# Optimization experiments

Hardware: AMD Instinct MI355X
Metric: run time of the kernel (lower is better)

Reference implementation:

```python
import jax, jax.numpy as jnp
import numpy as np

D_MODEL = 1024
N_HEADS = 16
HEAD_DIM = D_MODEL // N_HEADS  # 64
BATCH, SEQ = 2, 2048
MASK_FILL = -1000000000.0


def setup_inputs() -> dict:
    key = jax.random.key(0)
    ks = jax.random.split(key, 13)
    s = 1.0 / np.sqrt(D_MODEL)
    inp = {
        "q": jax.random.normal(ks[0], (BATCH, SEQ, D_MODEL), jnp.float32),
        "k": jax.random.normal(ks[1], (BATCH, SEQ, D_MODEL), jnp.float32),
        "v": jax.random.normal(ks[2], (BATCH, SEQ, D_MODEL), jnp.float32),
        "mask": jax.random.randint(ks[3], (BATCH, 1, SEQ, SEQ), 0, 2, jnp.int32),
        "Wq": jax.random.normal(ks[4], (D_MODEL, D_MODEL), jnp.float32) * s,
        "bq": jax.random.normal(ks[5], (D_MODEL,), jnp.float32) * s,
        "Wk": jax.random.normal(ks[6], (D_MODEL, D_MODEL), jnp.float32) * s,
        "bk": jax.random.normal(ks[7], (D_MODEL,), jnp.float32) * s,
        "Wv": jax.random.normal(ks[8], (D_MODEL, D_MODEL), jnp.float32) * s,
        "bv": jax.random.normal(ks[9], (D_MODEL,), jnp.float32) * s,
        "Wo": jax.random.normal(ks[10], (D_MODEL, D_MODEL), jnp.float32) * s,
        "bo": jax.random.normal(ks[11], (D_MODEL,), jnp.float32) * s,
    }
    return inp


def reference(q, k, v, mask, Wq, bq, Wk, bk, Wv, bv, Wo, bo):
    batch, seq, feat = q.shape
    # Linear projections (torch Linear: x @ W.T + b)
    qp = q @ Wq.T + bq
    kp = k @ Wk.T + bk
    vp = v @ Wv.T + bv

    def split(x):
        # (B, S, D) -> (B, H, S, Dh)
        return x.reshape(batch, seq, N_HEADS, HEAD_DIM).swapaxes(1, 2)

    qh, kh, vh = split(qp), split(kp), split(vp)

    # (B, H, S, S) score matrix, scaled
    score = jnp.einsum("bhqd,bhkd->bhqk", qh, kh) / jnp.sqrt(
        jnp.asarray(HEAD_DIM, qh.dtype))
    score = jnp.where(mask == 0, jnp.asarray(MASK_FILL, score.dtype), score)
    attn = jax.nn.softmax(score, axis=-1)
    out = jnp.einsum("bhqk,bhkd->bhqd", attn, vh)  # (B, H, S, Dh)
    joint = out.swapaxes(1, 2).reshape(batch, seq, feat)
    return joint @ Wo.T + bo
```

## Files before the change

kernel.cpp:

```cpp
#include <hip/hip_runtime.h>

typedef unsigned short u16;
typedef unsigned long long u64;
typedef float f32x4 __attribute__((ext_vector_type(4)));
typedef __bf16 bf16x4 __attribute__((ext_vector_type(4)));
typedef __bf16 bf16x8 __attribute__((ext_vector_type(8)));
typedef u16 u16x8 __attribute__((ext_vector_type(8)));

#define QSCALE 0.18033688011112042f

__device__ __forceinline__ u16 f2bf(float f) {
  unsigned int u = __float_as_uint(f);
  u += 0x7fffu + ((u >> 16) & 1u);
  return (u16)(u >> 16);
}

__device__ __forceinline__ void async16(const void* g, void* l) {
  __builtin_amdgcn_global_load_lds(
      (__attribute__((address_space(1))) void*)g,
      (__attribute__((address_space(3))) void*)l,
      16, 0, 0);
}

__device__ __forceinline__ f32x4 mfma16(bf16x8 a, bf16x8 b, f32x4 c) {
  return __builtin_amdgcn_mfma_f32_16x16x32_bf16(a, b, c, 0, 0, 0);
}

struct CvtArgs {
  const float* src[7];
  u16* dst[7];
};

__global__ __launch_bounds__(256) void cvt_kernel(CvtArgs a) {
  int z = blockIdx.z;
  int n = (z < 3) ? 4194304 : 1048576;
  int base = (blockIdx.x * 256 + threadIdx.x) * 8;
  if (base >= n) return;
  const float* s = a.src[z] + base;
  f32x4 x0 = *(const f32x4*)s;
  f32x4 x1 = *(const f32x4*)(s + 4);
  u16x8 pk;
  pk[0]=f2bf(x0[0]); pk[1]=f2bf(x0[1]); pk[2]=f2bf(x0[2]); pk[3]=f2bf(x0[3]);
  pk[4]=f2bf(x1[0]); pk[5]=f2bf(x1[1]); pk[6]=f2bf(x1[2]); pk[7]=f2bf(x1[3]);
  *(u16x8*)(a.dst[z] + base) = pk;
}

__global__ __launch_bounds__(256) void pack_mask_kernel(
    const int* __restrict__ mask, u64* __restrict__ pm) {
  int idx = blockIdx.x * 256 + threadIdx.x;
  const int4* src = (const int4*)(mask + (size_t)idx * 64);
  u64 bits = 0ull;
#pragma unroll
  for (int j = 0; j < 16; ++j) {
    int4 v = src[j];
    if (v.x) bits |= 1ull << (4 * j + 0);
    if (v.y) bits |= 1ull << (4 * j + 1);
    if (v.z) bits |= 1ull << (4 * j + 2);
    if (v.w) bits |= 1ull << (4 * j + 3);
  }
  pm[idx] = bits;
}

__device__ __forceinline__ void gemm_body(const u16* __restrict__ A,
                                          const u16* __restrict__ W,
                                          const float* __restrict__ bias,
                                          void* __restrict__ outraw, int mode,
                                          float oscale) {
  alignas(16) __shared__ u16 lA[128 * 32];
  alignas(16) __shared__ u16 lB[128 * 32];
  const int tid = threadIdx.x;
  const int lane = tid & 63, wv = tid >> 6;
  const int wm = wv >> 1, wn = wv & 1;
  const int m0 = blockIdx.y * 128, n0 = blockIdx.x * 128;
  const int l15 = lane & 15, quad = lane >> 4;
  const int srow = lane >> 2;
  const int scol = (lane & 3) * 8;

  f32x4 acc[4][4] = {};

  for (int k0 = 0; k0 < 1024; k0 += 32) {
#pragma unroll
    for (int t = 0; t < 2; ++t) {
      int rb = (wv * 2 + t) * 16;
      async16(A + (size_t)(m0 + rb + srow) * 1024 + k0 + scol, (char*)lA + rb * 64);
      async16(W + (size_t)(n0 + rb + srow) * 1024 + k0 + scol, (char*)lB + rb * 64);
    }
    __syncthreads();
    bf16x8 af[4], bfr[4];
#pragma unroll
    for (int i = 0; i < 4; ++i) {
      af[i]  = *(const bf16x8*)(lA + (wm * 64 + i * 16 + l15) * 32 + quad * 8);
      bfr[i] = *(const bf16x8*)(lB + (wn * 64 + i * 16 + l15) * 32 + quad * 8);
    }
#pragma unroll
    for (int i = 0; i < 4; ++i)
#pragma unroll
      for (int j = 0; j < 4; ++j)
        acc[i][j] = mfma16(af[i], bfr[j], acc[i][j]);
    __syncthreads();
  }

#pragma unroll
  for (int i = 0; i < 4; ++i) {
    int mbase = m0 + wm * 64 + i * 16 + quad * 4;
#pragma unroll
    for (int j = 0; j < 4; ++j) {
      int n = n0 + wn * 64 + j * 16 + l15;
      float bv = bias[n];
#pragma unroll
      for (int r = 0; r < 4; ++r) {
        int m = mbase + r;
        float val = (acc[i][j][r] + bv) * oscale;
        if (mode == 0) {
          int b = m >> 11, s = m & 2047, h = n >> 6, dh = n & 63;
          ((u16*)outraw)[((((size_t)b * 16 + h) * 2048 + s) << 6) + dh] = f2bf(val);
        } else if (mode == 1) {
          int b = m >> 11, s = m & 2047, h = n >> 6, dh = n & 63;
          ((u16*)outraw)[((((size_t)b * 16 + h) * 64 + dh) << 11) + s] = f2bf(val);
        } else {
          ((float*)outraw)[(size_t)m * 1024 + n] = val;
        }
      }
    }
  }
}

__global__ __launch_bounds__(256) void gemm_qkv_kernel(
    const u16* __restrict__ qb, const u16* __restrict__ kb, const u16* __restrict__ vb,
    const u16* __restrict__ Wqb, const float* __restrict__ bq,
    const u16* __restrict__ Wkb, const float* __restrict__ bk,
    const u16* __restrict__ Wvb, const float* __restrict__ bv,
    u16* __restrict__ qp, u16* __restrict__ kp, u16* __restrict__ vt) {
  if (blockIdx.z == 0)      gemm_body(qb, Wqb, bq, qp, 0, QSCALE);
  else if (blockIdx.z == 1) gemm_body(kb, Wkb, bk, kp, 0, 1.0f);
  else                      gemm_body(vb, Wvb, bv, vt, 1, 1.0f);
}

__global__ __launch_bounds__(256) void gemm_o_kernel(
    const u16* __restrict__ joint, const u16* __restrict__ Wob,
    const float* __restrict__ bo, float* __restrict__ out) {
  gemm_body(joint, Wob, bo, out, 2, 1.0f);
}

__global__ __launch_bounds__(256, 2) void attn_kernel(
    const u16* __restrict__ qp, const u16* __restrict__ kp,
    const u16* __restrict__ vt, const u64* __restrict__ pm,
    u16* __restrict__ joint) {
  alignas(16) __shared__ u16 kbuf[2][4096];
  alignas(16) __shared__ u16 vbuf[2][4096];
  alignas(16) __shared__ u16 pbuf[4][2][1024];

  const int tid = threadIdx.x, lane = tid & 63, wv = tid >> 6;
  const int quad = lane >> 4, l15 = lane & 15;
  const int q0 = blockIdx.x * 128;
  const int h = blockIdx.y, b = blockIdx.z;
  const size_t head_off = ((size_t)b * 16 + h) * 2048 * 64;
  const u16* Qh = qp + head_off;
  const u16* Kh = kp + head_off;
  const u16* Vh = vt + head_off;
  const int qr0 = q0 + wv * 32 + l15;
  const u64* pmq = pm + ((size_t)b * 2048 + qr0) * 32;

  bf16x8 qf[2][2];
#pragma unroll
  for (int g = 0; g < 2; ++g) {
    const u16* qrow = Qh + (size_t)(qr0 + g * 16) * 64 + quad * 8;
    qf[g][0] = *(const bf16x8*)(qrow);
    qf[g][1] = *(const bf16x8*)(qrow + 32);
  }

  const int sd0 = tid, sd1 = 256 + tid;
  const int snt0 = sd0 >> 7, shalf0 = (sd0 >> 6) & 1, sl60 = sd0 & 63;
  const int snt1 = sd1 >> 7, shalf1 = (sd1 >> 6) & 1, sl61 = sd1 & 63;
  const u16* kg0 = Kh + (size_t)(snt0 * 16 + (sl60 & 15)) * 64 + shalf0 * 32 + (sl60 >> 4) * 8;
  const u16* kg1 = Kh + (size_t)(snt1 * 16 + (sl61 & 15)) * 64 + shalf1 * 32 + (sl61 >> 4) * 8;
  const int vb0 = sd0 >> 6, vb1 = sd1 >> 6;
  const u16* vg0 = Vh + (size_t)((vb0 >> 1) * 16 + (sl60 & 15)) * 2048 + (vb0 & 1) * 32 + (sl60 >> 4) * 8;
  const u16* vg1 = Vh + (size_t)((vb1 >> 1) * 16 + (sl61 & 15)) * 2048 + (vb1 & 1) * 32 + (sl61 >> 4) * 8;

  f32x4 O[2][4] = {};
  f32x4 lacc[2] = {};
  const f32x4 fz = {};

  f32x4 SA[2][4], SB[2][4];
  bf16x8 vfA[8], vfB[8];
  u64 wA0, wA1, wB0, wB1;

#define SM_CHUNK(SP, WLO, WHI, g, nt)                                          \
  do {                                                                         \
    unsigned int hw_ = ((nt) < 2) ? (WLO) : (WHI);                             \
    unsigned int nib_ = hw_ >> (((nt) & 1) * 16 + quad * 4);                   \
    _Pragma("unroll") for (int r_ = 0; r_ < 4; ++r_) {                         \
      float pe_ = __builtin_amdgcn_exp2f(SP[g][nt][r_]);                       \
      SP[g][nt][r_] = ((nib_ >> r_) & 1u) ? pe_ : 0.f;                         \
    }                                                                          \
    lacc[g] += SP[g][nt];                                                      \
    bf16x4 pv_ = __builtin_convertvector(SP[g][nt], bf16x4);                   \
    int t4_ = 4 * (nt) + quad;                                                 \
    int ks_ = t4_ >> 3, qd_ = (t4_ & 7) >> 1;                                  \
    u16* pw_ = pbuf[wv][g] + ks_ * 512 + qd_ * 128 + l15 * 8 + (t4_ & 1) * 4;  \
    *(u64*)pw_ = *(const u64*)&pv_;                                            \
  } while (0)

#define ATTN_STEP(SC, SP, VC, VP, WC0, WC1, WP0, WP1, KT)                      \
  do {                                                                         \
    const int kt_ = (KT);                                                      \
    if (kt_ != 31) {                                                           \
      const size_t kadv_ = (size_t)(kt_ + 1) * 4096;                           \
      const int vadv_ = (kt_ + 1) * 64;                                        \
      char* kd_ = (char*)kbuf[(kt_ + 1) & 1];                                  \
      char* vd_ = (char*)vbuf[(kt_ + 1) & 1];                                  \
      async16(kg0 + kadv_, kd_ + sd0 * 16);                                    \
      async16(kg1 + kadv_, kd_ + sd1 * 16);                                    \
      async16(vg0 + vadv_, vd_ + sd0 * 16);                                    \
      async16(vg1 + vadv_, vd_ + sd1 * 16);                                    \
    }                                                                          \
    WC0 = pmq[kt_]; WC1 = pmq[kt_ + 512];                                      \
    const u16* kc_ = kbuf[kt_ & 1];                                            \
    const u16* vc_ = vbuf[kt_ & 1];                                            \
    unsigned int plo0_ = (unsigned int)(WP0), phi0_ = (unsigned int)((WP0) >> 32); \
    unsigned int plo1_ = (unsigned int)(WP1), phi1_ = (unsigned int)((WP1) >> 32); \
    _Pragma("unroll") for (int nt = 0; nt < 4; ++nt) {                         \
      bf16x8 k0_ = *(const bf16x8*)(kc_ + nt * 1024 + lane * 8);               \
      bf16x8 k1_ = *(const bf16x8*)(kc_ + nt * 1024 + 512 + lane * 8);         \
      f32x4 z0_ = mfma16(k0_, qf[0][0], fz);                                   \
      SC[0][nt] = mfma16(k1_, qf[0][1], z0_);                                  \
      f32x4 z1_ = mfma16(k0_, qf[1][0], fz);                                   \
      SC[1][nt] = mfma16(k1_, qf[1][1], z1_);                                  \
      SM_CHUNK(SP, plo0_, phi0_, 0, nt);                                       \
      SM_CHUNK(SP, plo1_, phi1_, 1, nt);                                       \
    }                                                                          \
    asm volatile("s_waitcnt lgkmcnt(0)" ::: "memory");                         \
    _Pragma("unroll") for (int ks = 0; ks < 2; ++ks) {                         \
      bf16x8 pf0_ = *(const bf16x8*)(pbuf[wv][0] + ks * 512 + lane * 8);       \
      bf16x8 pf1_ = *(const bf16x8*)(pbuf[wv][1] + ks * 512 + lane * 8);       \
      _Pragma("unroll") for (int nt = 0; nt < 4; ++nt) {                       \
        O[0][nt] = mfma16(VP[2 * nt + ks], pf0_, O[0][nt]);                    \
        O[1][nt] = mfma16(VP[2 * nt + ks], pf1_, O[1][nt]);                    \
      }                                                                        \
    }                                                                          \
    _Pragma("unroll") for (int nt = 0; nt < 4; ++nt) {                         \
      VC[2 * nt]     = *(const bf16x8*)(vc_ + (nt * 2) * 512 + lane * 8);      \
      VC[2 * nt + 1] = *(const bf16x8*)(vc_ + (nt * 2 + 1) * 512 + lane * 8);  \
    }                                                                          \
    __syncthreads();                                                           \
  } while (0)

  async16(kg0, (char*)kbuf[0] + sd0 * 16);
  async16(kg1, (char*)kbuf[0] + sd1 * 16);
  async16(vg0, (char*)vbuf[0] + sd0 * 16);
  async16(vg1, (char*)vbuf[0] + sd1 * 16);
  __syncthreads();

  async16(kg0 + 4096, (char*)kbuf[1] + sd0 * 16);
  async16(kg1 + 4096, (char*)kbuf[1] + sd1 * 16);
  async16(vg0 + 64,   (char*)vbuf[1] + sd0 * 16);
  async16(vg1 + 64,   (char*)vbuf[1] + sd1 * 16);

  wA0 = pmq[0]; wA1 = pmq[512];
#pragma unroll
  for (int nt = 0; nt < 4; ++nt) {
    bf16x8 k0_ = *(const bf16x8*)(kbuf[0] + nt * 1024 + lane * 8);
    bf16x8 k1_ = *(const bf16x8*)(kbuf[0] + nt * 1024 + 512 + lane * 8);
    f32x4 z0_ = mfma16(k0_, qf[0][0], fz);
    SA[0][nt] = mfma16(k1_, qf[0][1], z0_);
    f32x4 z1_ = mfma16(k0_, qf[1][0], fz);
    SA[1][nt] = mfma16(k1_, qf[1][1], z1_);
  }
#pragma unroll
  for (int nt = 0; nt < 4; ++nt) {
    vfA[2 * nt]     = *(const bf16x8*)(vbuf[0] + (nt * 2) * 512 + lane * 8);
    vfA[2 * nt + 1] = *(const bf16x8*)(vbuf[0] + (nt * 2 + 1) * 512 + lane * 8);
  }
  __syncthreads();

  for (int it = 0; it < 15; ++it) {
    ATTN_STEP(SB, SA, vfB, vfA, wB0, wB1, wA0, wA1, 2 * it + 1);
    ATTN_STEP(SA, SB, vfA, vfB, wA0, wA1, wB0, wB1, 2 * it + 2);
  }
  ATTN_STEP(SB, SA, vfB, vfA, wB0, wB1, wA0, wA1, 31);

  {
    unsigned int plo0_ = (unsigned int)wB0, phi0_ = (unsigned int)(wB0 >> 32);
    unsigned int plo1_ = (unsigned int)wB1, phi1_ = (unsigned int)(wB1 >> 32);
#pragma unroll
    for (int nt = 0; nt < 4; ++nt) {
      SM_CHUNK(SB, plo0_, phi0_, 0, nt);
      SM_CHUNK(SB, plo1_, phi1_, 1, nt);
    }
    asm volatile("s_waitcnt lgkmcnt(0)" ::: "memory");
#pragma unroll
    for (int ks = 0; ks < 2; ++ks) {
      bf16x8 pf0_ = *(const bf16x8*)(pbuf[wv][0] + ks * 512 + lane * 8);
      bf16x8 pf1_ = *(const bf16x8*)(pbuf[wv][1] + ks * 512 + lane * 8);
#pragma unroll
      for (int nt = 0; nt < 4; ++nt) {
        O[0][nt] = mfma16(vfB[2 * nt + ks], pf0_, O[0][nt]);
        O[1][nt] = mfma16(vfB[2 * nt + ks], pf1_, O[1][nt]);
      }
    }
  }

#undef ATTN_STEP
#undef SM_CHUNK

#pragma unroll
  for (int g = 0; g < 2; ++g) {
    float l = (lacc[g][0] + lacc[g][1]) + (lacc[g][2] + lacc[g][3]);
    l += __shfl_xor(l, 16, 64);
    l += __shfl_xor(l, 32, 64);
    float inv = 1.0f / l;
    size_t row_off = ((size_t)b * 2048 + qr0 + g * 16) * 1024 + h * 64;
#pragma unroll
    for (int nt = 0; nt < 4; ++nt) {
      f32x4 ov = O[g][nt] * inv;
      bf16x4 obv = __builtin_convertvector(ov, bf16x4);
      *(u64*)(joint + row_off + nt * 16 + quad * 4) = *(const u64*)&obv;
    }
  }
}

extern "C" void kernel_launch(void* const* d_in, const int* in_sizes, int n_in,
                              void* d_out, int out_size, void* d_ws, size_t ws_size,
                              hipStream_t stream) {
  const float* q  = (const float*)d_in[0];
  const float* k  = (const float*)d_in[1];
  const float* v  = (const float*)d_in[2];
  const int* mask = (const int*)d_in[3];
  const float* Wq = (const float*)d_in[4];
  const float* bq = (const float*)d_in[5];
  const float* Wk = (const float*)d_in[6];
  const float* bk = (const float*)d_in[7];
  const float* Wv = (const float*)d_in[8];
  const float* bv = (const float*)d_in[9];
  const float* Wo = (const float*)d_in[10];
  const float* bo = (const float*)d_in[11];
  float* out = (float*)d_out;

  u16* w = (u16*)d_ws;
  u16* qp    = w;
  u16* kp    = w + 4194304;
  u16* vt    = w + 8388608;
  u16* qb    = w + 12582912;
  u16* kb    = w + 16777216;
  u16* vb    = w + 20971520;
  u16* Wqb   = w + 25165824;
  u16* Wkb   = w + 26214400;
  u16* Wvb   = w + 27262976;
  u16* Wob   = w + 28311552;
  u64* pm    = (u64*)(w + 29360128);
  u16* joint = qb;

  CvtArgs ca;
  ca.src[0] = q;  ca.dst[0] = qb;
  ca.src[1] = k;  ca.dst[1] = kb;
  ca.src[2] = v;  ca.dst[2] = vb;
  ca.src[3] = Wq; ca.dst[3] = Wqb;
  ca.src[4] = Wk; ca.dst[4] = Wkb;
  ca.src[5] = Wv; ca.dst[5] = Wvb;
  ca.src[6] = Wo; ca.dst[6] = Wob;

  pack_mask_kernel<<<dim3(512), dim3(256), 0, stream>>>(mask, pm);
  cvt_kernel<<<dim3(2048, 1, 7), dim3(256), 0, stream>>>(ca);
  gemm_qkv_kernel<<<dim3(8, 32, 3), dim3(256), 0, stream>>>(
      qb, kb, vb, Wqb, bq, Wkb, bk, Wvb, bv, qp, kp, vt);
  attn_kernel<<<dim3(16, 16, 2), dim3(256), 0, stream>>>(qp, kp, vt, pm, joint);
  gemm_o_kernel<<<dim3(8, 32, 1), dim3(256), 0, stream>>>(joint, Wob, bo, out);
}
```

Before: 285.6 us.

## Load K/V fragments directly from global into registers, drop LDS staging and barriers

The attention kernel stops staging K and V tiles through shared memory with async global-to-LDS copies. Each wave now loads its own K and V MFMA fragments straight from global memory into registers, double-buffering K in registers, and the per-step __syncthreads is removed. This frees LDS and removes block-wide synchronisation, but each of the four waves now fetches the same K/V data separately. That multiplies global/L2 traffic, and V loads are strided by rows of 2048, which risks exposed load latency.

Result: slower. 348.7 us (+22.1%).

```diff
diff --git a/kernel.cpp b/kernel.cpp
--- a/kernel.cpp
+++ b/kernel.cpp
@@ -146,8 +146,6 @@
     const u16* __restrict__ qp, const u16* __restrict__ kp,
     const u16* __restrict__ vt, const u64* __restrict__ pm,
     u16* __restrict__ joint) {
-  alignas(16) __shared__ u16 kbuf[2][4096];
-  alignas(16) __shared__ u16 vbuf[2][4096];
   alignas(16) __shared__ u16 pbuf[4][2][1024];
 
   const int tid = threadIdx.x, lane = tid & 63, wv = tid >> 6;
@@ -169,124 +167,111 @@
     qf[g][1] = *(const bf16x8*)(qrow + 32);
   }
 
-  const int sd0 = tid, sd1 = 256 + tid;
-  const int snt0 = sd0 >> 7, shalf0 = (sd0 >> 6) & 1, sl60 = sd0 & 63;
-  const int snt1 = sd1 >> 7, shalf1 = (sd1 >> 6) & 1, sl61 = sd1 & 63;
-  const u16* kg0 = Kh + (size_t)(snt0 * 16 + (sl60 & 15)) * 64 + shalf0 * 32 + (sl60 >> 4) * 8;
-  const u16* kg1 = Kh + (size_t)(snt1 * 16 + (sl61 & 15)) * 64 + shalf1 * 32 + (sl61 >> 4) * 8;
-  const int vb0 = sd0 >> 6, vb1 = sd1 >> 6;
-  const u16* vg0 = Vh + (size_t)((vb0 >> 1) * 16 + (sl60 & 15)) * 2048 + (vb0 & 1) * 32 + (sl60 >> 4) * 8;
-  const u16* vg1 = Vh + (size_t)((vb1 >> 1) * 16 + (sl61 & 15)) * 2048 + (vb1 & 1) * 32 + (sl61 >> 4) * 8;
+  const u16* kbase = Kh + (size_t)l15 * 64 + quad * 8;
+  const u16* vbase = Vh + (size_t)l15 * 2048 + quad * 8;
 
   f32x4 O[2][4] = {};
   f32x4 lacc[2] = {};
   const f32x4 fz = {};
 
-  f32x4 SA[2][4], SB[2][4];
-  bf16x8 vfA[8], vfB[8];
-  u64 wA0, wA1, wB0, wB1;
-
-#define SM_CHUNK(SP, WLO, WHI, g, nt)                                          \
+  f32x4 S[2][4];
+  bf16x8 kfA[8], kfB[8];
+  bf16x8 vf[8];
+  u64 wP0, wP1, wC0, wC1;
+
+#define SM_CHUNK(WLO, WHI, g, nt)                                              \
   do {                                                                         \
     unsigned int hw_ = ((nt) < 2) ? (WLO) : (WHI);                             \
     unsigned int nib_ = hw_ >> (((nt) & 1) * 16 + quad * 4);                   \
     _Pragma("unroll") for (int r_ = 0; r_ < 4; ++r_) {                         \
-      float pe_ = __builtin_amdgcn_exp2f(SP[g][nt][r_]);                       \
-      SP[g][nt][r_] = ((nib_ >> r_) & 1u) ? pe_ : 0.f;                         \
-    }                                                                          \
-    lacc[g] += SP[g][nt];                                                      \
-    bf16x4 pv_ = __builtin_convertvector(SP[g][nt], bf16x4);                   \
+      float pe_ = __builtin_amdgcn_exp2f(S[g][nt][r_]);                        \
+      S[g][nt][r_] = ((nib_ >> r_) & 1u) ? pe_ : 0.f;                          \
+    }                                                                          \
+    lacc[g] += S[g][nt];                                                       \
+    bf16x4 pv_ = __builtin_convertvector(S[g][nt], bf16x4);                    \
     int t4_ = 4 * (nt) + quad;                                                 \
     int ks_ = t4_ >> 3, qd_ = (t4_ & 7) >> 1;                                  \
     u16* pw_ = pbuf[wv][g] + ks_ * 512 + qd_ * 128 + l15 * 8 + (t4_ & 1) * 4;  \
     *(u64*)pw_ = *(const u64*)&pv_;                                            \
   } while (0)
 
-#define ATTN_STEP(SC, SP, VC, VP, WC0, WC1, WP0, WP1, KT)                      \
+#define ATTN_STEP(KFC, KFN, KT)                                                \
   do {                                                                         \
     const int kt_ = (KT);                                                      \
     if (kt_ != 31) {                                                           \
-      const size_t kadv_ = (size_t)(kt_ + 1) * 4096;                           \
-      const int vadv_ = (kt_ + 1) * 64;                                        \
-      char* kd_ = (char*)kbuf[(kt_ + 1) & 1];                                  \
-      char* vd_ = (char*)vbuf[(kt_ + 1) & 1];                                  \
-      async16(kg0 + kadv_, kd_ + sd0 * 16);                                    \
-      async16(kg1 + kadv_, kd_ + sd1 * 16);                                    \
-      async16(vg0 + vadv_, vd_ + sd0 * 16);                                    \
-      async16(vg1 + vadv_, vd_ + sd1 * 16);                                    \
-    }                                                                          \
-    WC0 = pmq[kt_]; WC1 = pmq[kt_ + 512];                                      \
-    const u16* kc_ = kbuf[kt_ & 1];                                            \
-    const u16* vc_ = vbuf[kt_ & 1];                                            \
-    unsigned int plo0_ = (unsigned int)(WP0), phi0_ = (unsigned int)((WP0) >> 32); \
-    unsigned int plo1_ = (unsigned int)(WP1), phi1_ = (unsigned int)((WP1) >> 32); \
+      const u16* kn_ = kbase + (size_t)(kt_ + 1) * 4096;                       \
+      _Pragma("unroll") for (int nt = 0; nt < 4; ++nt) {                       \
+        KFN[2 * nt]     = *(const bf16x8*)(kn_ + nt * 1024);                   \
+        KFN[2 * nt + 1] = *(const bf16x8*)(kn_ + nt * 1024 + 32);              \
+      }                                                                        \
+    }                                                                          \
+    wC0 = pmq[kt_]; wC1 = pmq[kt_ + 512];                                      \
+    unsigned int plo0_ = (unsigned int)wP0, phi0_ = (unsigned int)(wP0 >> 32); \
+    unsigned int plo1_ = (unsigned int)wP1, phi1_ = (unsigned int)(wP1 >> 32); \
     _Pragma("unroll") for (int nt = 0; nt < 4; ++nt) {                         \
-      bf16x8 k0_ = *(const bf16x8*)(kc_ + nt * 1024 + lane * 8);               \
-      bf16x8 k1_ = *(const bf16x8*)(kc_ + nt * 1024 + 512 + lane * 8);         \
-      f32x4 z0_ = mfma16(k0_, qf[0][0], fz);                                   \
-      SC[0][nt] = mfma16(k1_, qf[0][1], z0_);                                  \
-      f32x4 z1_ = mfma16(k0_, qf[1][0], fz);                                   \
-      SC[1][nt] = mfma16(k1_, qf[1][1], z1_);                                  \
-      SM_CHUNK(SP, plo0_, phi0_, 0, nt);                                       \
-      SM_CHUNK(SP, plo1_, phi1_, 1, nt);                                       \
+      SM_CHUNK(plo0_, phi0_, 0, nt);                                           \
+      SM_CHUNK(plo1_, phi1_, 1, nt);                                           \
+      f32x4 z0_ = mfma16(KFC[2 * nt], qf[0][0], fz);                           \
+      S[0][nt] = mfma16(KFC[2 * nt + 1], qf[0][1], z0_);                       \
+      f32x4 z1_ = mfma16(KFC[2 * nt], qf[1][0], fz);                           \
+      S[1][nt] = mfma16(KFC[2 * nt + 1], qf[1][1], z1_);                       \
     }                                                                          \
     asm volatile("s_waitcnt lgkmcnt(0)" ::: "memory");                         \
     _Pragma("unroll") for (int ks = 0; ks < 2; ++ks) {                         \
       bf16x8 pf0_ = *(const bf16x8*)(pbuf[wv][0] + ks * 512 + lane * 8);       \
       bf16x8 pf1_ = *(const bf16x8*)(pbuf[wv][1] + ks * 512 + lane * 8);       \
       _Pragma("unroll") for (int nt = 0; nt < 4; ++nt) {                       \
-        O[0][nt] = mfma16(VP[2 * nt + ks], pf0_, O[0][nt]);                    \
-        O[1][nt] = mfma16(VP[2 * nt + ks], pf1_, O[1][nt]);                    \
+        O[0][nt] = mfma16(vf[2 * nt + ks], pf0_, O[0][nt]);                    \
+        O[1][nt] = mfma16(vf[2 * nt + ks], pf1_, O[1][nt]);                    \
       }                                                                        \
     }                                                                          \
-    _Pragma("unroll") for (int nt = 0; nt < 4; ++nt) {                         \
-      VC[2 * nt]     = *(const bf16x8*)(vc_ + (nt * 2) * 512 + lane * 8);      \
-      VC[2 * nt + 1] = *(const bf16x8*)(vc_ + (nt * 2 + 1) * 512 + lane * 8);  \
-    }                                                                          \
-    __syncthreads();                                                           \
+    {                                                                          \
+      const u16* vn_ = vbase + (size_t)kt_ * 64;                               \
+      _Pragma("unroll") for (int nt = 0; nt < 4; ++nt) {                       \
+        vf[2 * nt]     = *(const bf16x8*)(vn_ + nt * 32768);                   \
+        vf[2 * nt + 1] = *(const bf16x8*)(vn_ + nt * 32768 + 32);              \
+      }                                                                        \
+    }                                                                          \
+    wP0 = wC0; wP1 = wC1;                                                      \
   } while (0)
 
-  async16(kg0, (char*)kbuf[0] + sd0 * 16);
-  async16(kg1, (char*)kbuf[0] + sd1 * 16);
-  async16(vg0, (char*)vbuf[0] + sd0 * 16);
-  async16(vg1, (char*)vbuf[0] + sd1 * 16);
-  __syncthreads();
-
-  async16(kg0 + 4096, (char*)kbuf[1] + sd0 * 16);
-  async16(kg1 + 4096, (char*)kbuf[1] + sd1 * 16);
-  async16(vg0 + 64,   (char*)vbuf[1] + sd0 * 16);
-  async16(vg1 + 64,   (char*)vbuf[1] + sd1 * 16);
-
-  wA0 = pmq[0]; wA1 = pmq[512];
 #pragma unroll
   for (int nt = 0; nt < 4; ++nt) {
-    bf16x8 k0_ = *(const bf16x8*)(kbuf[0] + nt * 1024 + lane * 8);
-    bf16x8 k1_ = *(const bf16x8*)(kbuf[0] + nt * 1024 + 512 + lane * 8);
-    f32x4 z0_ = mfma16(k0_, qf[0][0], fz);
-    SA[0][nt] = mfma16(k1_, qf[0][1], z0_);
-    f32x4 z1_ = mfma16(k0_, qf[1][0], fz);
-    SA[1][nt] = mfma16(k1_, qf[1][1], z1_);
-  }
+    kfA[2 * nt]     = *(const bf16x8*)(kbase + nt * 1024);
+    kfA[2 * nt + 1] = *(const bf16x8*)(kbase + nt * 1024 + 32);
+  }
+  wP0 = pmq[0]; wP1 = pmq[512];
 #pragma unroll
   for (int nt = 0; nt < 4; ++nt) {
-    vfA[2 * nt]     = *(const bf16x8*)(vbuf[0] + (nt * 2) * 512 + lane * 8);
-    vfA[2 * nt + 1] = *(const bf16x8*)(vbuf[0] + (nt * 2 + 1) * 512 + lane * 8);
-  }
-  __syncthreads();
+    f32x4 z0 = mfma16(kfA[2 * nt], qf[0][0], fz);
+    S[0][nt] = mfma16(kfA[2 * nt + 1], qf[0][1], z0);
+    f32x4 z1 = mfma16(kfA[2 * nt], qf[1][0], fz);
+    S[1][nt] = mfma16(kfA[2 * nt + 1], qf[1][1], z1);
+  }
+#pragma unroll
+  for (int nt = 0; nt < 4; ++nt) {
+    kfB[2 * nt]     = *(const bf16x8*)(kbase + 4096 + nt * 1024);
+    kfB[2 * nt + 1] = *(const bf16x8*)(kbase + 4096 + nt * 1024 + 32);
+  }
+#pragma unroll
+  for (int nt = 0; nt < 4; ++nt) {
+    vf[2 * nt]     = *(const bf16x8*)(vbase + nt * 32768);
+    vf[2 * nt + 1] = *(const bf16x8*)(vbase + nt * 32768 + 32);
+  }
 
   for (int it = 0; it < 15; ++it) {
-    ATTN_STEP(SB, SA, vfB, vfA, wB0, wB1, wA0, wA1, 2 * it + 1);
-    ATTN_STEP(SA, SB, vfA, vfB, wA0, wA1, wB0, wB1, 2 * it + 2);
-  }
-  ATTN_STEP(SB, SA, vfB, vfA, wB0, wB1, wA0, wA1, 31);
+    ATTN_STEP(kfB, kfA, 2 * it + 1);
+    ATTN_STEP(kfA, kfB, 2 * it + 2);
+  }
+  ATTN_STEP(kfB, kfA, 31);
 
   {
-    unsigned int plo0_ = (unsigned int)wB0, phi0_ = (unsigned int)(wB0 >> 32);
-    unsigned int plo1_ = (unsigned int)wB1, phi1_ = (unsigned int)(wB1 >> 32);
+    unsigned int plo0_ = (unsigned int)wP0, phi0_ = (unsigned int)(wP0 >> 32);
+    unsigned int plo1_ = (unsigned int)wP1, phi1_ = (unsigned int)(wP1 >> 32);
 #pragma unroll
     for (int nt = 0; nt < 4; ++nt) {
-      SM_CHUNK(SB, plo0_, phi0_, 0, nt);
-      SM_CHUNK(SB, plo1_, phi1_, 1, nt);
+      SM_CHUNK(plo0_, phi0_, 0, nt);
+      SM_CHUNK(plo1_, phi1_, 1, nt);
     }
     asm volatile("s_waitcnt lgkmcnt(0)" ::: "memory");
 #pragma unroll
@@ -295,8 +280,8 @@
       bf16x8 pf1_ = *(const bf16x8*)(pbuf[wv][1] + ks * 512 + lane * 8);
 #pragma unroll
       for (int nt = 0; nt < 4; ++nt) {
-        O[0][nt] = mfma16(vfB[2 * nt + ks], pf0_, O[0][nt]);
-        O[1][nt] = mfma16(vfB[2 * nt + ks], pf1_, O[1][nt]);
+        O[0][nt] = mfma16(vf[2 * nt + ks], pf0_, O[0][nt]);
+        O[1][nt] = mfma16(vf[2 * nt + ks], pf1_, O[1][nt]);
       }
     }
   }
```
